# Performance work log

Measured on AMD Instinct MI355X. Metric: run time of the kernel, lower is better.

## Reference

```python
import jax, jax.numpy as jnp
import numpy as np

B, DL, DC, DG = 4, 64, 64, 64
NL, NC = 8192, 16384
SLOPE = 0.01  # LeakyReLU default negative_slope


def _lin(x, W, b):
    # 1x1 Conv1d == per-node linear: x [B, in, N] -> [B, out, N]
    return jnp.einsum('oi,bin->bon', W, x) + b[None, :, None]


def _leaky(x):
    return jnp.where(x >= 0, x, SLOPE * x)


def _flip(L):
    # swap first and second half along last dim (literal <-> complement)
    n = L.shape[-1]
    return jnp.concatenate([L[..., n // 2:], L[..., :n // 2]], axis=-1)


def setup_inputs() -> dict:
    key = jax.random.key(0)
    ks = jax.random.split(key, 14)
    L_t = jax.random.normal(ks[0], (B, DL, NL), dtype=jnp.float32)
    C_t = jax.random.normal(ks[1], (B, DC, NC), dtype=jnp.float32)
    U_t = jax.random.normal(ks[2], (B, DG, 1), dtype=jnp.float32)
    # sparse 0/1 adjacency, ~8 literals per clause
    A = (jax.random.uniform(ks[3], (NC, NL)) < 0.001).astype(jnp.float32)
    A_t = A.T
    s = 0.05
    W_Lmsg = s * jax.random.normal(ks[4], (DC, DL));      b_Lmsg = jnp.zeros((DC,))
    W_Cmsg = s * jax.random.normal(ks[5], (DL, DC));      b_Cmsg = jnp.zeros((DL,))
    W_Lu   = s * jax.random.normal(ks[6], (DL, 3 * DL));  b_Lu   = jnp.zeros((DL,))
    W_Cu   = s * jax.random.normal(ks[7], (DC, 2 * DC));  b_Cu   = jnp.zeros((DC,))
    W_Uu   = s * jax.random.normal(ks[8], (DG, DL + DC + DG)); b_Uu = jnp.zeros((DG,))
    return dict(L_t=L_t, C_t=C_t, U_t=U_t, A=A, A_t=A_t,
                W_Lmsg=W_Lmsg, b_Lmsg=b_Lmsg, W_Cmsg=W_Cmsg, b_Cmsg=b_Cmsg,
                W_Lu=W_Lu, b_Lu=b_Lu, W_Cu=W_Cu, b_Cu=b_Cu, W_Uu=W_Uu, b_Uu=b_Uu)


def reference(L_t, C_t, U_t, A, A_t,
              W_Lmsg, b_Lmsg, W_Cmsg, b_Cmsg,
              W_Lu, b_Lu, W_Cu, b_Cu, W_Uu, b_Uu):
    # literal -> clause messages: [B, d_c, n_lits] @ [n_lits, n_clauses]
    M_l = _lin(L_t, W_Lmsg, b_Lmsg) @ A_t
    C_t_new = _leaky(_lin(jnp.concatenate([C_t, M_l], axis=1), W_Cu, b_Cu))
    # clause -> literal messages: [B, d_l, n_clauses] @ [n_clauses, n_lits]
    M_c = _lin(C_t_new, W_Cmsg, b_Cmsg) @ A
    L_t_new = _leaky(_lin(jnp.concatenate([L_t, M_c, _flip(L_t)], axis=1), W_Lu, b_Lu))
    glob = jnp.concatenate([L_t_new.sum(-1, keepdims=True),
                            C_t_new.sum(-1, keepdims=True), U_t], axis=1)
    U_t_new = _leaky(_lin(glob, W_Uu, b_Uu))
    return (L_t_new, C_t_new, U_t_new)
```

## Files before the change

kernel.cpp:

```cpp
#include <hip/hip_runtime.h>

#define NLIT 8192
#define NCLS 16384
#define BATCH 4
#define DD 64
#define CCAP 64
#define LCAP 64

__device__ __forceinline__ float leaky(float x){ return x >= 0.f ? x : 0.01f*x; }

__global__ __launch_bounds__(256) void extract_k(const float* __restrict__ A,
    int* __restrict__ ccnt, int* __restrict__ clist,
    int* __restrict__ lcnt, int* __restrict__ llist){
  const int total4 = NCLS * (NLIT/4);
  int stride = gridDim.x * blockDim.x;
  for (int i = blockIdx.x*blockDim.x + threadIdx.x; i < total4; i += stride){
    float4 v = ((const float4*)A)[i];
    if (v.x!=0.f || v.y!=0.f || v.z!=0.f || v.w!=0.f){
      int c = i >> 11;
      int l = (i & 2047) << 2;
      float vv[4] = {v.x, v.y, v.z, v.w};
      #pragma unroll
      for (int j=0;j<4;j++){
        if (vv[j]!=0.f){
          int p = atomicAdd(&ccnt[c],1);
          if (p < CCAP) clist[c*CCAP+p] = l+j;
          int q = atomicAdd(&lcnt[l+j],1);
          if (q < LCAP) llist[(l+j)*LCAP+q] = c;
        }
      }
    }
  }
}

__global__ __launch_bounds__(256) void lmsg_k(const float* __restrict__ L,
    const float* __restrict__ W, const float* __restrict__ bias, float* __restrict__ LmsgT){
  __shared__ float X[64][65];
  __shared__ float Y[64][65];
  int b  = blockIdx.x >> 7;
  int l0 = (blockIdx.x & 127) << 6;
  int lane = threadIdx.x & 63;
  int wg = __builtin_amdgcn_readfirstlane(threadIdx.x >> 6);
  const float* Lb = L + (size_t)b*DD*NLIT;
  #pragma unroll
  for (int r=0;r<16;r++){
    int i = wg + 4*r;
    X[lane][i] = Lb[(size_t)i*NLIT + l0 + lane];
  }
  __syncthreads();
  float acc[16];
  #pragma unroll
  for (int j=0;j<16;j++) acc[j] = bias[wg*16+j];
  #pragma unroll 4
  for (int i=0;i<64;i++){
    float x = X[lane][i];
    #pragma unroll
    for (int j=0;j<16;j++) acc[j] += W[(wg*16+j)*64+i] * x;
  }
  #pragma unroll
  for (int j=0;j<16;j++) Y[lane][wg*16+j] = acc[j];
  __syncthreads();
  float* out = LmsgT + ((size_t)b*NLIT + l0)*64;
  #pragma unroll
  for (int r=0;r<16;r++){
    int cc = wg + 4*r;
    out[cc*64 + lane] = Y[cc][lane];
  }
}

__device__ __forceinline__ float gather_sum(const float* __restrict__ src,
    const int* __restrict__ list, int k, int lane){
  float acc = 0.f;
  int j = 0;
  for (; j+4 <= k; j += 4){
    int4 li = *(const int4*)&list[j];
    float a0 = src[(size_t)li.x*64 + lane];
    float a1 = src[(size_t)li.y*64 + lane];
    float a2 = src[(size_t)li.z*64 + lane];
    float a3 = src[(size_t)li.w*64 + lane];
    acc += (a0 + a1) + (a2 + a3);
  }
  for (; j < k; j++) acc += src[(size_t)list[j]*64 + lane];
  return acc;
}

__global__ __launch_bounds__(256) void clause_k(const float* __restrict__ Ct,
    const float* __restrict__ LmsgT, const int* __restrict__ ccnt, const int* __restrict__ clist,
    const float* __restrict__ W_Cu, const float* __restrict__ b_Cu,
    const float* __restrict__ W_Cmsg, const float* __restrict__ b_Cmsg,
    float* __restrict__ CmsgT, float* __restrict__ outC){
  __shared__ float SA[64][65];
  __shared__ float SB[64][65];
  int b  = blockIdx.x >> 8;
  int c0 = (blockIdx.x & 255) << 6;
  int lane = threadIdx.x & 63;
  int wg = __builtin_amdgcn_readfirstlane(threadIdx.x >> 6);
  int kk[16];
  #pragma unroll
  for (int t=0;t<16;t++){
    int k = ccnt[c0 + wg*16 + t];
    kk[t] = k > CCAP ? CCAP : k;
  }
  const float* Cb = Ct + (size_t)b*DD*NCLS;
  #pragma unroll
  for (int r=0;r<16;r++){
    int i = wg + 4*r;
    SA[lane][i] = Cb[(size_t)i*NCLS + c0 + lane];
  }
  const float* Lm = LmsgT + (size_t)b*NLIT*64;
  #pragma unroll 2
  for (int t=0;t<16;t++){
    int cc = wg*16 + t;
    int c  = c0 + cc;
    SB[cc][lane] = gather_sum(Lm, &clist[c*CCAP], kk[t], lane);
  }
  __syncthreads();
  float v[16];
  {
    float acc[16];
    #pragma unroll
    for (int j=0;j<16;j++) acc[j] = b_Cu[wg*16+j];
    #pragma unroll 4
    for (int i=0;i<64;i++){
      float xa = SA[lane][i];
      float xm = SB[lane][i];
      #pragma unroll
      for (int j=0;j<16;j++){
        int o = wg*16+j;
        acc[j] += W_Cu[o*128+i]*xa + W_Cu[o*128+64+i]*xm;
      }
    }
    #pragma unroll
    for (int j=0;j<16;j++) v[j] = leaky(acc[j]);
  }
  float* oC = outC + (size_t)b*DD*NCLS;
  #pragma unroll
  for (int j=0;j<16;j++){
    int o = wg*16+j;
    oC[(size_t)o*NCLS + c0 + lane] = v[j];
  }
  __syncthreads();
  #pragma unroll
  for (int j=0;j<16;j++) SB[lane][wg*16+j] = v[j];
  __syncthreads();
  float acc2[16];
  #pragma unroll
  for (int j=0;j<16;j++) acc2[j] = b_Cmsg[wg*16+j];
  #pragma unroll 4
  for (int i=0;i<64;i++){
    float x = SB[lane][i];
    #pragma unroll
    for (int j=0;j<16;j++) acc2[j] += W_Cmsg[(wg*16+j)*64+i]*x;
  }
  #pragma unroll
  for (int j=0;j<16;j++) SA[lane][wg*16+j] = acc2[j];
  __syncthreads();
  float* oM = CmsgT + ((size_t)b*NCLS + c0)*64;
  #pragma unroll
  for (int r=0;r<16;r++){
    int cc = wg + 4*r;
    oM[cc*64 + lane] = SA[cc][lane];
  }
}

__global__ __launch_bounds__(256) void literal_k(const float* __restrict__ Lt,
    const float* __restrict__ CmsgT, const int* __restrict__ lcnt, const int* __restrict__ llist,
    const float* __restrict__ W_Lu, const float* __restrict__ b_Lu,
    float* __restrict__ outL){
  __shared__ float SX[64][65];
  __shared__ float SF[64][65];
  __shared__ float SM[64][65];
  int b  = blockIdx.x >> 7;
  int l0 = (blockIdx.x & 127) << 6;
  int lane = threadIdx.x & 63;
  int wg = __builtin_amdgcn_readfirstlane(threadIdx.x >> 6);
  int kk[16];
  #pragma unroll
  for (int t=0;t<16;t++){
    int k = lcnt[l0 + wg*16 + t];
    kk[t] = k > LCAP ? LCAP : k;
  }
  const float* Lb = Lt + (size_t)b*DD*NLIT;
  int f0 = l0 ^ 4096;
  #pragma unroll
  for (int r=0;r<16;r++){
    int i = wg + 4*r;
    SX[lane][i] = Lb[(size_t)i*NLIT + l0 + lane];
    SF[lane][i] = Lb[(size_t)i*NLIT + f0 + lane];
  }
  const float* Cm = CmsgT + (size_t)b*NCLS*64;
  #pragma unroll 2
  for (int t=0;t<16;t++){
    int cc = wg*16 + t;
    int l  = l0 + cc;
    SM[cc][lane] = gather_sum(Cm, &llist[l*LCAP], kk[t], lane);
  }
  __syncthreads();
  float acc[16];
  #pragma unroll
  for (int j=0;j<16;j++) acc[j] = b_Lu[wg*16+j];
  #pragma unroll 4
  for (int i=0;i<64;i++){
    float xx = SX[lane][i], xm = SM[lane][i], xf = SF[lane][i];
    #pragma unroll
    for (int j=0;j<16;j++){
      int o = wg*16+j;
      acc[j] += W_Lu[o*192+i]*xx + W_Lu[o*192+64+i]*xm + W_Lu[o*192+128+i]*xf;
    }
  }
  float* oL = outL + (size_t)b*DD*NLIT;
  #pragma unroll
  for (int j=0;j<16;j++){
    int o = wg*16+j;
    oL[(size_t)o*NLIT + l0 + lane] = leaky(acc[j]);
  }
}

__global__ __launch_bounds__(256) void reduce_k(const float* __restrict__ outL,
    const float* __restrict__ outC, float* __restrict__ Lsum, float* __restrict__ Csum){
  __shared__ float red[4];
  int r = blockIdx.x;
  int t = threadIdx.x;
  float s = 0.f;
  if (r < 256){
    const float4* p = (const float4*)(outC + (size_t)r*NCLS);
    #pragma unroll
    for (int i=0;i<16;i++){
      float4 v = p[t + 256*i];
      s += v.x + v.y + v.z + v.w;
    }
  } else {
    const float4* p = (const float4*)(outL + (size_t)(r-256)*NLIT);
    #pragma unroll
    for (int i=0;i<8;i++){
      float4 v = p[t + 256*i];
      s += v.x + v.y + v.z + v.w;
    }
  }
  #pragma unroll
  for (int sft=32;sft>0;sft>>=1) s += __shfl_xor(s, sft, 64);
  if ((t & 63) == 0) red[t >> 6] = s;
  __syncthreads();
  if (t == 0){
    float tot = red[0] + red[1] + red[2] + red[3];
    if (r < 256) Csum[r] = tot; else Lsum[r-256] = tot;
  }
}

__global__ void u_k(const float* __restrict__ Lsum, const float* __restrict__ Csum,
                    const float* __restrict__ Ut, const float* __restrict__ W,
                    const float* __restrict__ bias, float* __restrict__ outU){
  int t = threadIdx.x;
  int b = t >> 6, o = t & 63;
  float acc = bias[o];
  for (int i=0;i<64;i++){
    acc += W[o*192+i]*Lsum[b*64+i] + W[o*192+64+i]*Csum[b*64+i] + W[o*192+128+i]*Ut[b*64+i];
  }
  outU[t] = leaky(acc);
}

extern "C" void kernel_launch(void* const* d_in, const int* in_sizes, int n_in,
                              void* d_out, int out_size, void* d_ws, size_t ws_size,
                              hipStream_t stream){
  (void)in_sizes; (void)n_in; (void)out_size; (void)ws_size;
  const float* L_t    = (const float*)d_in[0];
  const float* C_t    = (const float*)d_in[1];
  const float* U_t    = (const float*)d_in[2];
  const float* A      = (const float*)d_in[3];
  const float* W_Lmsg = (const float*)d_in[5];
  const float* b_Lmsg = (const float*)d_in[6];
  const float* W_Cmsg = (const float*)d_in[7];
  const float* b_Cmsg = (const float*)d_in[8];
  const float* W_Lu   = (const float*)d_in[9];
  const float* b_Lu   = (const float*)d_in[10];
  const float* W_Cu   = (const float*)d_in[11];
  const float* b_Cu   = (const float*)d_in[12];
  const float* W_Uu   = (const float*)d_in[13];
  const float* b_Uu   = (const float*)d_in[14];

  char* ws = (char*)d_ws;
  float* LmsgT = (float*)ws;
  float* CmsgT = (float*)(ws + 8388608);
  int*   ccnt  = (int*)  (ws + 25165824);
  int*   lcnt  = (int*)  (ws + 25231360);
  float* Lsum  = (float*)(ws + 25264128);
  float* Csum  = (float*)(ws + 25265152);
  int*   clist = (int*)  (ws + 25266176);
  int*   llist = (int*)  (ws + 29460480);

  hipMemsetAsync(ws + 25165824, 0, 98304, stream);

  float* outL = (float*)d_out;
  float* outC = (float*)d_out + 2097152;
  float* outU = (float*)d_out + 6291456;

  extract_k<<<16384, 256, 0, stream>>>(A, ccnt, clist, lcnt, llist);
  lmsg_k   <<<512,   256, 0, stream>>>(L_t, W_Lmsg, b_Lmsg, LmsgT);
  clause_k <<<1024,  256, 0, stream>>>(C_t, LmsgT, ccnt, clist, W_Cu, b_Cu,
                                       W_Cmsg, b_Cmsg, CmsgT, outC);
  literal_k<<<512,   256, 0, stream>>>(L_t, CmsgT, lcnt, llist, W_Lu, b_Lu, outL);
  reduce_k <<<512,   256, 0, stream>>>(outL, outC, Lsum, Csum);
  u_k      <<<1,     256, 0, stream>>>(Lsum, Csum, U_t, W_Uu, b_Uu, outU);
}
```

Before: 1.099 ms.

## Vectorize neighbor gathers with padded lists and unroll adjacency scan

The adjacency scan now has each thread issue 8 independent 16-byte loads up front and tests them with integer ORs instead of running a grid-stride float loop. A new pad kernel clamps the counts and pads the neighbor lists to multiples of four with a sentinel index. That index points to an extra zero row appended to the message buffers. The gather then loads float4 per lane and handles four neighbors per round using lane groups, reducing with cross-lane shuffles. This replaces a scalar-per-lane loop with a tail, at the cost of one extra kernel launch and shuffle overhead.

```diff
diff --git a/kernel.cpp b/kernel.cpp
--- a/kernel.cpp
+++ b/kernel.cpp
@@ -6,23 +6,29 @@
 #define DD 64
 #define CCAP 64
 #define LCAP 64
+#define LSTRIDE (NLIT + 1)
+#define CSTRIDE (NCLS + 1)
 
 __device__ __forceinline__ float leaky(float x){ return x >= 0.f ? x : 0.01f*x; }
 
-__global__ __launch_bounds__(256) void extract_k(const float* __restrict__ A,
+__global__ __launch_bounds__(256) void extract_k(const uint4* __restrict__ A4,
     int* __restrict__ ccnt, int* __restrict__ clist,
     int* __restrict__ lcnt, int* __restrict__ llist){
-  const int total4 = NCLS * (NLIT/4);
-  int stride = gridDim.x * blockDim.x;
-  for (int i = blockIdx.x*blockDim.x + threadIdx.x; i < total4; i += stride){
-    float4 v = ((const float4*)A)[i];
-    if (v.x!=0.f || v.y!=0.f || v.z!=0.f || v.w!=0.f){
+  const int T = 16384*256;
+  int tid = blockIdx.x*256 + threadIdx.x;
+  uint4 v[8];
+  #pragma unroll
+  for (int u=0;u<8;u++) v[u] = A4[tid + (size_t)u*T];
+  #pragma unroll
+  for (int u=0;u<8;u++){
+    if (v[u].x | v[u].y | v[u].z | v[u].w){
+      int i = tid + u*T;
       int c = i >> 11;
       int l = (i & 2047) << 2;
-      float vv[4] = {v.x, v.y, v.z, v.w};
+      unsigned vv[4] = {v[u].x, v[u].y, v[u].z, v[u].w};
       #pragma unroll
       for (int j=0;j<4;j++){
-        if (vv[j]!=0.f){
+        if (vv[j]){
           int p = atomicAdd(&ccnt[c],1);
           if (p < CCAP) clist[c*CCAP+p] = l+j;
           int q = atomicAdd(&lcnt[l+j],1);
@@ -30,6 +36,29 @@
         }
       }
     }
+  }
+}
+
+__global__ __launch_bounds__(256) void pad_k(int* __restrict__ ccnt, int* __restrict__ clist,
+    int* __restrict__ lcnt, int* __restrict__ llist,
+    float* __restrict__ LmsgT, float* __restrict__ CmsgT){
+  int tid = blockIdx.x*256 + threadIdx.x;
+  if (tid < NCLS){
+    int k = ccnt[tid]; if (k > CCAP) k = CCAP;
+    ccnt[tid] = k;
+    int e = (k+3) & ~3; if (e > CCAP) e = CCAP;
+    for (int j=k;j<e;j++) clist[tid*CCAP+j] = NLIT;
+  } else {
+    int l = tid - NCLS;
+    int k = lcnt[l]; if (k > LCAP) k = LCAP;
+    lcnt[l] = k;
+    int e = (k+3) & ~3; if (e > LCAP) e = LCAP;
+    for (int j=k;j<e;j++) llist[l*LCAP+j] = NCLS;
+  }
+  if (tid < 256){
+    int b = tid >> 6, f = tid & 63;
+    LmsgT[((size_t)b*LSTRIDE + NLIT)*64 + f] = 0.f;
+    CmsgT[((size_t)b*CSTRIDE + NCLS)*64 + f] = 0.f;
   }
 }
 
@@ -60,7 +89,7 @@
   #pragma unroll
   for (int j=0;j<16;j++) Y[lane][wg*16+j] = acc[j];
   __syncthreads();
-  float* out = LmsgT + ((size_t)b*NLIT + l0)*64;
+  float* out = LmsgT + ((size_t)b*LSTRIDE + l0)*64;
   #pragma unroll
   for (int r=0;r<16;r++){
     int cc = wg + 4*r;
@@ -68,20 +97,24 @@
   }
 }
 
-__device__ __forceinline__ float gather_sum(const float* __restrict__ src,
-    const int* __restrict__ list, int k, int lane){
-  float acc = 0.f;
-  int j = 0;
-  for (; j+4 <= k; j += 4){
-    int4 li = *(const int4*)&list[j];
-    float a0 = src[(size_t)li.x*64 + lane];
-    float a1 = src[(size_t)li.y*64 + lane];
-    float a2 = src[(size_t)li.z*64 + lane];
-    float a3 = src[(size_t)li.w*64 + lane];
-    acc += (a0 + a1) + (a2 + a3);
-  }
-  for (; j < k; j++) acc += src[(size_t)list[j]*64 + lane];
-  return acc;
+__device__ __forceinline__ void gather4(const float* __restrict__ src,
+    const int* __restrict__ list, int k, int lane, float* __restrict__ sbrow){
+  int g = lane >> 4;
+  int h = lane & 15;
+  float4 acc = {0.f,0.f,0.f,0.f};
+  int rounds = (k + 3) >> 2;
+  for (int r = 0; r < rounds; r++){
+    int4 li = *(const int4*)&list[4*r];
+    int idx = g==0 ? li.x : (g==1 ? li.y : (g==2 ? li.z : li.w));
+    float4 v = *(const float4*)&src[(size_t)idx*64 + 4*h];
+    acc.x += v.x; acc.y += v.y; acc.z += v.z; acc.w += v.w;
+  }
+  acc.x += __shfl_xor(acc.x, 16, 64); acc.y += __shfl_xor(acc.y, 16, 64);
+  acc.z += __shfl_xor(acc.z, 16, 64); acc.w += __shfl_xor(acc.w, 16, 64);
+  acc.x += __shfl_xor(acc.x, 32, 64); acc.y += __shfl_xor(acc.y, 32, 64);
+  acc.z += __shfl_xor(acc.z, 32, 64); acc.w += __shfl_xor(acc.w, 32, 64);
+  float val = g==0 ? acc.x : (g==1 ? acc.y : (g==2 ? acc.z : acc.w));
+  sbrow[4*h + g] = val;
 }
 
 __global__ __launch_bounds__(256) void clause_k(const float* __restrict__ Ct,
@@ -107,12 +140,11 @@
     int i = wg + 4*r;
     SA[lane][i] = Cb[(size_t)i*NCLS + c0 + lane];
   }
-  const float* Lm = LmsgT + (size_t)b*NLIT*64;
+  const float* Lm = LmsgT + (size_t)b*LSTRIDE*64;
   #pragma unroll 2
   for (int t=0;t<16;t++){
     int cc = wg*16 + t;
-    int c  = c0 + cc;
-    SB[cc][lane] = gather_sum(Lm, &clist[c*CCAP], kk[t], lane);
+    gather4(Lm, &clist[(c0+cc)*CCAP], kk[t], lane, &SB[cc][0]);
   }
   __syncthreads();
   float v[16];
@@ -155,7 +187,7 @@
   #pragma unroll
   for (int j=0;j<16;j++) SA[lane][wg*16+j] = acc2[j];
   __syncthreads();
-  float* oM = CmsgT + ((size_t)b*NCLS + c0)*64;
+  float* oM = CmsgT + ((size_t)b*CSTRIDE + c0)*64;
   #pragma unroll
   for (int r=0;r<16;r++){
     int cc = wg + 4*r;
@@ -188,12 +220,11 @@
     SX[lane][i] = Lb[(size_t)i*NLIT + l0 + lane];
     SF[lane][i] = Lb[(size_t)i*NLIT + f0 + lane];
   }
-  const float* Cm = CmsgT + (size_t)b*NCLS*64;
+  const float* Cm = CmsgT + (size_t)b*CSTRIDE*64;
   #pragma unroll 2
   for (int t=0;t<16;t++){
     int cc = wg*16 + t;
-    int l  = l0 + cc;
-    SM[cc][lane] = gather_sum(Cm, &llist[l*LCAP], kk[t], lane);
+    gather4(Cm, &llist[(l0+cc)*LCAP], kk[t], lane, &SM[cc][0]);
   }
   __syncthreads();
   float acc[16];
@@ -280,21 +311,22 @@
 
   char* ws = (char*)d_ws;
   float* LmsgT = (float*)ws;
-  float* CmsgT = (float*)(ws + 8388608);
-  int*   ccnt  = (int*)  (ws + 25165824);
-  int*   lcnt  = (int*)  (ws + 25231360);
-  float* Lsum  = (float*)(ws + 25264128);
-  float* Csum  = (float*)(ws + 25265152);
-  int*   clist = (int*)  (ws + 25266176);
-  int*   llist = (int*)  (ws + 29460480);
-
-  hipMemsetAsync(ws + 25165824, 0, 98304, stream);
+  float* CmsgT = (float*)(ws + 8389632);
+  int*   ccnt  = (int*)  (ws + 25167872);
+  int*   lcnt  = (int*)  (ws + 25233408);
+  float* Lsum  = (float*)(ws + 25266176);
+  float* Csum  = (float*)(ws + 25267200);
+  int*   clist = (int*)  (ws + 25268224);
+  int*   llist = (int*)  (ws + 29462528);
+
+  hipMemsetAsync(ws + 25167872, 0, 98304, stream);
 
   float* outL = (float*)d_out;
   float* outC = (float*)d_out + 2097152;
   float* outU = (float*)d_out + 6291456;
 
-  extract_k<<<16384, 256, 0, stream>>>(A, ccnt, clist, lcnt, llist);
+  extract_k<<<16384, 256, 0, stream>>>((const uint4*)A, ccnt, clist, lcnt, llist);
+  pad_k    <<<96,    256, 0, stream>>>(ccnt, clist, lcnt, llist, LmsgT, CmsgT);
   lmsg_k   <<<512,   256, 0, stream>>>(L_t, W_Lmsg, b_Lmsg, LmsgT);
   clause_k <<<1024,  256, 0, stream>>>(C_t, LmsgT, ccnt, clist, W_Cu, b_Cu,
                                        W_Cmsg, b_Cmsg, CmsgT, outC);
```

After: 1.109 ms. About the same (+0.9%).

## Fuse extract with lmsg, reduce with literal, and vectorize neighbor gathers

Applied to the files above, without the earlier changes.

Merges adjacency extraction and the literal message projection into one launch, and merges the clause-sum reduction into the literal kernel, so fewer kernels launch and independent work overlaps. Extraction now issues eight 16-byte loads per thread and tests nonzero with integer ORs. The per-row gather is replaced by a 4-row grouped float4 gather with shuffle reductions, meant to give more memory-level parallelism. In exchange the code is more complex, and wave divergence across the four rows of a group wastes lanes.

```diff
diff --git a/kernel.cpp b/kernel.cpp
--- a/kernel.cpp
+++ b/kernel.cpp
@@ -2,86 +2,114 @@
 
 #define NLIT 8192
 #define NCLS 16384
-#define BATCH 4
 #define DD 64
 #define CCAP 64
 #define LCAP 64
 
 __device__ __forceinline__ float leaky(float x){ return x >= 0.f ? x : 0.01f*x; }
 
-__global__ __launch_bounds__(256) void extract_k(const float* __restrict__ A,
+__device__ __forceinline__ int sel4(int g, int4 li){
+  return g==0 ? li.x : (g==1 ? li.y : (g==2 ? li.z : li.w));
+}
+
+__global__ __launch_bounds__(256) void extract_lmsg_k(const uint4* __restrict__ A4,
     int* __restrict__ ccnt, int* __restrict__ clist,
-    int* __restrict__ lcnt, int* __restrict__ llist){
-  const int total4 = NCLS * (NLIT/4);
-  int stride = gridDim.x * blockDim.x;
-  for (int i = blockIdx.x*blockDim.x + threadIdx.x; i < total4; i += stride){
-    float4 v = ((const float4*)A)[i];
-    if (v.x!=0.f || v.y!=0.f || v.z!=0.f || v.w!=0.f){
-      int c = i >> 11;
-      int l = (i & 2047) << 2;
-      float vv[4] = {v.x, v.y, v.z, v.w};
-      #pragma unroll
-      for (int j=0;j<4;j++){
-        if (vv[j]!=0.f){
-          int p = atomicAdd(&ccnt[c],1);
-          if (p < CCAP) clist[c*CCAP+p] = l+j;
-          int q = atomicAdd(&lcnt[l+j],1);
-          if (q < LCAP) llist[(l+j)*LCAP+q] = c;
+    int* __restrict__ lcnt, int* __restrict__ llist,
+    const float* __restrict__ L, const float* __restrict__ W,
+    const float* __restrict__ bias, float* __restrict__ LmsgT){
+  if (blockIdx.x < 16384){
+    const int T = 16384*256;
+    int tid = blockIdx.x*256 + threadIdx.x;
+    uint4 v[8];
+    #pragma unroll
+    for (int u=0;u<8;u++) v[u] = A4[tid + (size_t)u*T];
+    #pragma unroll
+    for (int u=0;u<8;u++){
+      if (v[u].x | v[u].y | v[u].z | v[u].w){
+        int i = tid + u*T;
+        int c = i >> 11;
+        int l = (i & 2047) << 2;
+        unsigned vv[4] = {v[u].x, v[u].y, v[u].z, v[u].w};
+        #pragma unroll
+        for (int j=0;j<4;j++){
+          if (vv[j]){
+            int p = atomicAdd(&ccnt[c],1);
+            if (p < CCAP) clist[c*CCAP+p] = l+j;
+            int q = atomicAdd(&lcnt[l+j],1);
+            if (q < LCAP) llist[(l+j)*LCAP+q] = c;
+          }
         }
       }
     }
-  }
-}
-
-__global__ __launch_bounds__(256) void lmsg_k(const float* __restrict__ L,
-    const float* __restrict__ W, const float* __restrict__ bias, float* __restrict__ LmsgT){
-  __shared__ float X[64][65];
-  __shared__ float Y[64][65];
-  int b  = blockIdx.x >> 7;
-  int l0 = (blockIdx.x & 127) << 6;
-  int lane = threadIdx.x & 63;
-  int wg = __builtin_amdgcn_readfirstlane(threadIdx.x >> 6);
-  const float* Lb = L + (size_t)b*DD*NLIT;
-  #pragma unroll
-  for (int r=0;r<16;r++){
-    int i = wg + 4*r;
-    X[lane][i] = Lb[(size_t)i*NLIT + l0 + lane];
-  }
-  __syncthreads();
-  float acc[16];
-  #pragma unroll
-  for (int j=0;j<16;j++) acc[j] = bias[wg*16+j];
-  #pragma unroll 4
-  for (int i=0;i<64;i++){
-    float x = X[lane][i];
-    #pragma unroll
-    for (int j=0;j<16;j++) acc[j] += W[(wg*16+j)*64+i] * x;
-  }
-  #pragma unroll
-  for (int j=0;j<16;j++) Y[lane][wg*16+j] = acc[j];
-  __syncthreads();
-  float* out = LmsgT + ((size_t)b*NLIT + l0)*64;
-  #pragma unroll
-  for (int r=0;r<16;r++){
-    int cc = wg + 4*r;
-    out[cc*64 + lane] = Y[cc][lane];
-  }
-}
-
-__device__ __forceinline__ float gather_sum(const float* __restrict__ src,
-    const int* __restrict__ list, int k, int lane){
-  float acc = 0.f;
-  int j = 0;
-  for (; j+4 <= k; j += 4){
-    int4 li = *(const int4*)&list[j];
-    float a0 = src[(size_t)li.x*64 + lane];
-    float a1 = src[(size_t)li.y*64 + lane];
-    float a2 = src[(size_t)li.z*64 + lane];
-    float a3 = src[(size_t)li.w*64 + lane];
-    acc += (a0 + a1) + (a2 + a3);
-  }
-  for (; j < k; j++) acc += src[(size_t)list[j]*64 + lane];
-  return acc;
+  } else {
+    __shared__ float X[64][65];
+    __shared__ float Y[64][65];
+    int bid = blockIdx.x - 16384;
+    int b  = bid >> 7;
+    int l0 = (bid & 127) << 6;
+    int lane = threadIdx.x & 63;
+    int wg = __builtin_amdgcn_readfirstlane(threadIdx.x >> 6);
+    const float* Lb = L + (size_t)b*DD*NLIT;
+    #pragma unroll
+    for (int r=0;r<16;r++){
+      int i = wg + 4*r;
+      X[lane][i] = Lb[(size_t)i*NLIT + l0 + lane];
+    }
+    __syncthreads();
+    float acc[16];
+    #pragma unroll
+    for (int j=0;j<16;j++) acc[j] = bias[wg*16+j];
+    #pragma unroll 4
+    for (int i=0;i<64;i++){
+      float x = X[lane][i];
+      #pragma unroll
+      for (int j=0;j<16;j++) acc[j] += W[(wg*16+j)*64+i] * x;
+    }
+    #pragma unroll
+    for (int j=0;j<16;j++) Y[lane][wg*16+j] = acc[j];
+    __syncthreads();
+    float* out = LmsgT + ((size_t)b*NLIT + l0)*64;
+    #pragma unroll
+    for (int r=0;r<16;r++){
+      int cc = wg + 4*r;
+      out[cc*64 + lane] = Y[cc][lane];
+    }
+  }
+}
+
+__device__ __forceinline__ void gather_grp4(const float* __restrict__ src,
+    const int* __restrict__ list, int cap, const int* kk, int lane,
+    float (* __restrict__ sb)[65], int row0){
+  int g = lane >> 4;
+  int h = lane & 15;
+  float4 a0={0.f,0.f,0.f,0.f}, a1=a0, a2=a0, a3=a0;
+  int r0=(kk[0]+3)>>2, r1=(kk[1]+3)>>2, r2=(kk[2]+3)>>2, r3=(kk[3]+3)>>2;
+  int Rm = max(max(r0,r1),max(r2,r3));
+  for (int r=0;r<Rm;r++){
+    if (r<r0){ int4 li=*(const int4*)&list[0*cap+4*r]; int e=4*r+g; bool vd=e<kk[0];
+      int idx=vd?sel4(g,li):0; float4 x=*(const float4*)&src[(size_t)idx*64+4*h];
+      if(vd){ a0.x+=x.x; a0.y+=x.y; a0.z+=x.z; a0.w+=x.w; } }
+    if (r<r1){ int4 li=*(const int4*)&list[1*cap+4*r]; int e=4*r+g; bool vd=e<kk[1];
+      int idx=vd?sel4(g,li):0; float4 x=*(const float4*)&src[(size_t)idx*64+4*h];
+      if(vd){ a1.x+=x.x; a1.y+=x.y; a1.z+=x.z; a1.w+=x.w; } }
+    if (r<r2){ int4 li=*(const int4*)&list[2*cap+4*r]; int e=4*r+g; bool vd=e<kk[2];
+      int idx=vd?sel4(g,li):0; float4 x=*(const float4*)&src[(size_t)idx*64+4*h];
+      if(vd){ a2.x+=x.x; a2.y+=x.y; a2.z+=x.z; a2.w+=x.w; } }
+    if (r<r3){ int4 li=*(const int4*)&list[3*cap+4*r]; int e=4*r+g; bool vd=e<kk[3];
+      int idx=vd?sel4(g,li):0; float4 x=*(const float4*)&src[(size_t)idx*64+4*h];
+      if(vd){ a3.x+=x.x; a3.y+=x.y; a3.z+=x.z; a3.w+=x.w; } }
+  }
+  #pragma unroll
+  for (int s=16;s<=32;s<<=1){
+    a0.x+=__shfl_xor(a0.x,s,64); a0.y+=__shfl_xor(a0.y,s,64); a0.z+=__shfl_xor(a0.z,s,64); a0.w+=__shfl_xor(a0.w,s,64);
+    a1.x+=__shfl_xor(a1.x,s,64); a1.y+=__shfl_xor(a1.y,s,64); a1.z+=__shfl_xor(a1.z,s,64); a1.w+=__shfl_xor(a1.w,s,64);
+    a2.x+=__shfl_xor(a2.x,s,64); a2.y+=__shfl_xor(a2.y,s,64); a2.z+=__shfl_xor(a2.z,s,64); a2.w+=__shfl_xor(a2.w,s,64);
+    a3.x+=__shfl_xor(a3.x,s,64); a3.y+=__shfl_xor(a3.y,s,64); a3.z+=__shfl_xor(a3.z,s,64); a3.w+=__shfl_xor(a3.w,s,64);
+  }
+  sb[row0+0][4*h+g] = g==0?a0.x:(g==1?a0.y:(g==2?a0.z:a0.w));
+  sb[row0+1][4*h+g] = g==0?a1.x:(g==1?a1.y:(g==2?a1.z:a1.w));
+  sb[row0+2][4*h+g] = g==0?a2.x:(g==1?a2.y:(g==2?a2.z:a2.w));
+  sb[row0+3][4*h+g] = g==0?a3.x:(g==1?a3.y:(g==2?a3.z:a3.w));
 }
 
 __global__ __launch_bounds__(256) void clause_k(const float* __restrict__ Ct,
@@ -108,11 +136,10 @@
     SA[lane][i] = Cb[(size_t)i*NCLS + c0 + lane];
   }
   const float* Lm = LmsgT + (size_t)b*NLIT*64;
-  #pragma unroll 2
-  for (int t=0;t<16;t++){
-    int cc = wg*16 + t;
-    int c  = c0 + cc;
-    SB[cc][lane] = gather_sum(Lm, &clist[c*CCAP], kk[t], lane);
+  #pragma unroll
+  for (int tg=0;tg<4;tg++){
+    int row0 = wg*16 + tg*4;
+    gather_grp4(Lm, &clist[(c0+row0)*CCAP], CCAP, &kk[tg*4], lane, SB, row0);
   }
   __syncthreads();
   float v[16];
@@ -163,10 +190,28 @@
   }
 }
 
-__global__ __launch_bounds__(256) void literal_k(const float* __restrict__ Lt,
+__global__ __launch_bounds__(256) void literal_redc_k(const float* __restrict__ Lt,
     const float* __restrict__ CmsgT, const int* __restrict__ lcnt, const int* __restrict__ llist,
     const float* __restrict__ W_Lu, const float* __restrict__ b_Lu,
-    float* __restrict__ outL){
+    float* __restrict__ outL, const float* __restrict__ outC, float* __restrict__ Csum){
+  if (blockIdx.x >= 512){
+    __shared__ float red[4];
+    int r = blockIdx.x - 512;
+    int t = threadIdx.x;
+    float s = 0.f;
+    const float4* p = (const float4*)(outC + (size_t)r*NCLS);
+    #pragma unroll
+    for (int i=0;i<16;i++){
+      float4 v = p[t + 256*i];
+      s += v.x + v.y + v.z + v.w;
+    }
+    #pragma unroll
+    for (int sft=32;sft>0;sft>>=1) s += __shfl_xor(s, sft, 64);
+    if ((t & 63) == 0) red[t >> 6] = s;
+    __syncthreads();
+    if (t == 0) Csum[r] = red[0] + red[1] + red[2] + red[3];
+    return;
+  }
   __shared__ float SX[64][65];
   __shared__ float SF[64][65];
   __shared__ float SM[64][65];
@@ -189,11 +234,10 @@
     SF[lane][i] = Lb[(size_t)i*NLIT + f0 + lane];
   }
   const float* Cm = CmsgT + (size_t)b*NCLS*64;
-  #pragma unroll 2
-  for (int t=0;t<16;t++){
-    int cc = wg*16 + t;
-    int l  = l0 + cc;
-    SM[cc][lane] = gather_sum(Cm, &llist[l*LCAP], kk[t], lane);
+  #pragma unroll
+  for (int tg=0;tg<4;tg++){
+    int row0 = wg*16 + tg*4;
+    gather_grp4(Cm, &llist[(l0+row0)*LCAP], LCAP, &kk[tg*4], lane, SM, row0);
   }
   __syncthreads();
   float acc[16];
@@ -216,35 +260,23 @@
   }
 }
 
-__global__ __launch_bounds__(256) void reduce_k(const float* __restrict__ outL,
-    const float* __restrict__ outC, float* __restrict__ Lsum, float* __restrict__ Csum){
+__global__ __launch_bounds__(256) void redl_k(const float* __restrict__ outL,
+    float* __restrict__ Lsum){
   __shared__ float red[4];
   int r = blockIdx.x;
   int t = threadIdx.x;
   float s = 0.f;
-  if (r < 256){
-    const float4* p = (const float4*)(outC + (size_t)r*NCLS);
-    #pragma unroll
-    for (int i=0;i<16;i++){
-      float4 v = p[t + 256*i];
-      s += v.x + v.y + v.z + v.w;
-    }
-  } else {
-    const float4* p = (const float4*)(outL + (size_t)(r-256)*NLIT);
-    #pragma unroll
-    for (int i=0;i<8;i++){
-      float4 v = p[t + 256*i];
-      s += v.x + v.y + v.z + v.w;
-    }
+  const float4* p = (const float4*)(outL + (size_t)r*NLIT);
+  #pragma unroll
+  for (int i=0;i<8;i++){
+    float4 v = p[t + 256*i];
+    s += v.x + v.y + v.z + v.w;
   }
   #pragma unroll
   for (int sft=32;sft>0;sft>>=1) s += __shfl_xor(s, sft, 64);
   if ((t & 63) == 0) red[t >> 6] = s;
   __syncthreads();
-  if (t == 0){
-    float tot = red[0] + red[1] + red[2] + red[3];
-    if (r < 256) Csum[r] = tot; else Lsum[r-256] = tot;
-  }
+  if (t == 0) Lsum[r] = red[0] + red[1] + red[2] + red[3];
 }
 
 __global__ void u_k(const float* __restrict__ Lsum, const float* __restrict__ Csum,
@@ -294,11 +326,12 @@
   float* outC = (float*)d_out + 2097152;
   float* outU = (float*)d_out + 6291456;
 
-  extract_k<<<16384, 256, 0, stream>>>(A, ccnt, clist, lcnt, llist);
-  lmsg_k   <<<512,   256, 0, stream>>>(L_t, W_Lmsg, b_Lmsg, LmsgT);
-  clause_k <<<1024,  256, 0, stream>>>(C_t, LmsgT, ccnt, clist, W_Cu, b_Cu,
-                                       W_Cmsg, b_Cmsg, CmsgT, outC);
-  literal_k<<<512,   256, 0, stream>>>(L_t, CmsgT, lcnt, llist, W_Lu, b_Lu, outL);
-  reduce_k <<<512,   256, 0, stream>>>(outL, outC, Lsum, Csum);
-  u_k      <<<1,     256, 0, stream>>>(Lsum, Csum, U_t, W_Uu, b_Uu, outU);
-}
+  extract_lmsg_k<<<16896, 256, 0, stream>>>((const uint4*)A, ccnt, clist, lcnt, llist,
+                                            L_t, W_Lmsg, b_Lmsg, LmsgT);
+  clause_k      <<<1024,  256, 0, stream>>>(C_t, LmsgT, ccnt, clist, W_Cu, b_Cu,
+                                            W_Cmsg, b_Cmsg, CmsgT, outC);
+  literal_redc_k<<<768,   256, 0, stream>>>(L_t, CmsgT, lcnt, llist, W_Lu, b_Lu,
+                                            outL, outC, Csum);
+  redl_k        <<<256,   256, 0, stream>>>(outL, Lsum);
+  u_k           <<<1,     256, 0, stream>>>(Lsum, Csum, U_t, W_Uu, b_Uu, outU);
+}
```

Measured after the change: 1.089 ms. No clear change (-0.8%).
